# Optimization experiments

Measured on AMD Instinct MI355X. Metric: run time of the kernel, lower is better.

## Reference

```python
import jax, jax.numpy as jnp
import numpy as np

M, TS, NX, NY = 24, 60, 192, 192   # solutions, source timesteps, source grid
H, D = 4, 8                         # num_heads, d_head
SIGMA = 0.2
N_TIME_STEPS = 50
T_MAX = 200.0
LX = 100.0                          # solutions[0]['params']['Lx']
SRC_T_MAX = 200.0                   # solutions[0]['params']['t_max']
NG = 50                             # target grid resolution (hard-coded in source)


def setup_inputs():
    key = jax.random.key(0)
    ks = jax.random.split(key, 8)
    c1_preds = jax.random.normal(ks[0], (M, TS, NX, NY), jnp.float32)
    c2_preds = jax.random.normal(ks[1], (M, TS, NX, NY), jnp.float32)
    lys = 30.0 + 90.0 * jax.random.uniform(ks[2], (M,), jnp.float32)
    c_cus = 0.0029 * jax.random.uniform(ks[3], (M,), jnp.float32)
    c_nis = 0.0018 * jax.random.uniform(ks[4], (M,), jnp.float32)
    params = jnp.stack([lys, c_cus, c_nis], axis=1)  # [M,3]
    # nonuniform, sorted per-solution y grid spanning [0, Ly_m]
    base = jnp.linspace(0.0, 1.0, NY, dtype=jnp.float32) ** 1.2
    src_y = lys[:, None] * base[None, :]  # [M,NY]
    src_t_last = 100.0 + 200.0 * jax.random.uniform(ks[5], (M,), jnp.float32)
    Wq = 0.3 * jax.random.normal(ks[6], (3, H * D), jnp.float32)
    Wk = 0.3 * jax.random.normal(ks[7], (3, H * D), jnp.float32)
    bq = jnp.zeros((H * D,), jnp.float32)
    bk = jnp.zeros((H * D,), jnp.float32)
    return dict(c1_preds=c1_preds, c2_preds=c2_preds, params=params, src_y=src_y,
                src_t_last=src_t_last, Wq=Wq, bq=bq, Wk=Wk, bk=bk,
                ly_target=jnp.float32(75.0), c_cu_target=jnp.float32(0.0015),
                c_ni_target=jnp.float32(0.0009))


def _axis_interp(grid, q):
    """1-D linear interp setup. grid [G] sorted, q [P] -> (idx, frac, in_bounds)."""
    G = grid.shape[-1]
    idx = jnp.clip(jnp.searchsorted(grid, q, side='right') - 1, 0, G - 2)
    g0 = jnp.take(grid, idx)
    g1 = jnp.take(grid, idx + 1)
    frac = (q - g0) / (g1 - g0)
    inb = (q >= grid[0]) & (q <= grid[-1])  # scipy fill_value=0 outside
    return idx, frac, inb


def reference(c1_preds, c2_preds, params, src_y, src_t_last, Wq, bq, Wk, bk,
              ly_target, c_cu_target, c_ni_target):
    lys, c_cus, c_nis = params[:, 0], params[:, 1], params[:, 2]
    # normalization exactly as in the torch forward
    ly_n = (lys - 30.0) / (120.0 - 30.0)
    cu_n = c_cus / 0.0029
    ni_n = c_nis / 0.0018
    t_ly = (ly_target - 30.0) / (120.0 - 30.0)
    t_cu = c_cu_target / 0.0029
    t_ni = c_ni_target / 0.0018

    p = jnp.stack([ly_n, cu_n, ni_n], axis=1)            # [M,3]
    tgt = jnp.stack([t_ly, t_cu, t_ni])[None, :]          # [1,3]
    Q = (tgt @ Wq + bq).reshape(H, D)                     # [H,D]
    K = (p @ Wk + bk).reshape(-1, H, D)                   # [M,H,D]
    logits = jnp.einsum('mhd,hd->mh', K, Q) / jnp.sqrt(jnp.float32(D))
    attn = jax.nn.softmax(logits, axis=0).mean(axis=1)    # softmax over solutions, mean heads -> [M]

    dist2 = ((ly_n - t_ly) ** 2 + (cu_n - t_cu) ** 2 + (ni_n - t_ni) ** 2) / SIGMA ** 2
    sw = jnp.exp(-dist2 / 2.0)
    sw = sw / (sw.sum() + 1e-12)
    w = attn * sw
    w = w / (w.sum() + 1e-12)
    w = jax.lax.stop_gradient(w)  # original detaches weights before interpolation

    # ---- physics-aware interpolation ----
    times = jnp.linspace(0.0, min(SRC_T_MAX, T_MAX), N_TIME_STEPS)  # [T]
    ti = jnp.clip(jnp.round(times[:, None] / src_t_last[None, :] * (TS - 1)).astype(jnp.int32),
                  0, TS - 1)                                         # [T,M]

    src_x = jnp.linspace(0.0, LX, NX)
    qx = jnp.linspace(0.0, LX, NG)
    qy = (jnp.arange(NG, dtype=jnp.float32) / (NG - 1)) * ly_target  # linspace(0, ly_target, NG)

    ix, fx, mx = _axis_interp(src_x, qx)                             # [NG] each (shared x grid)
    scale = ly_target / lys                                           # [M]
    y_scaled = src_y * scale[:, None]                                 # [M,NY]
    iy, fy, my = jax.vmap(lambda g: _axis_interp(g, qy))(y_scaled)    # [M,NG] each
    mask = (mx[None, :, None] & my[:, None, :]).astype(c1_preds.dtype)  # [M,NG,NG]

    T = N_TIME_STEPS
    iy_b = jnp.broadcast_to(iy[None, :, None, :], (T, M, NG, NG))
    iy1_b = jnp.broadcast_to((iy + 1)[None, :, None, :], (T, M, NG, NG))

    def interp_field(preds):
        vals = preds[jnp.arange(M)[None, :], ti]                      # [T,M,NX,NY] time gather
        fxc = fx[None, None, :, None]
        vx = vals[:, :, ix, :] * (1.0 - fxc) + vals[:, :, ix + 1, :] * fxc  # [T,M,NG,NY]
        v0 = jnp.take_along_axis(vx, iy_b, axis=3)                    # [T,M,NG,NG]
        v1 = jnp.take_along_axis(vx, iy1_b, axis=3)
        fyc = fy[None, :, None, :]
        v = (v0 * (1.0 - fyc) + v1 * fyc) * mask[None]
        return jnp.einsum('tmij,m->tij', v, w)                        # weighted sum over solutions

    c1 = interp_field(c1_preds).at[:, :, 0].set(c_cu_target)
    c2 = interp_field(c2_preds).at[:, :, -1].set(c_ni_target)
    return jnp.stack([c1, c2])  # [2, T, NG, NG]
```

## Files before the change

kernel.cpp:

```cpp
#include <hip/hip_runtime.h>
#include <math.h>

#define M   24
#define TS  60
#define NX  192
#define NY  192
#define H_  4
#define D_  8
#define NTS 50
#define NG  50

__device__ float g_w[M];
__device__ int   g_ti[NTS][M];
__device__ int   g_ix[NG];
__device__ float g_fx[NG];
__device__ float g_mx[NG];
__device__ int   g_iy[M][NG];
__device__ float g_fy[M][NG];
__device__ float g_my[M][NG];

__global__ __launch_bounds__(256) void prep_kernel(
    const float* __restrict__ params, const float* __restrict__ src_y,
    const float* __restrict__ stl,
    const float* __restrict__ Wq, const float* __restrict__ bq,
    const float* __restrict__ Wk, const float* __restrict__ bk,
    const float* __restrict__ lyt_p, const float* __restrict__ ccu_p,
    const float* __restrict__ cni_p)
{
    const int tid = threadIdx.x;
    __shared__ float s_logits[M][H_];
    __shared__ float s_sw[M];

    const float ly_target = lyt_p[0];
    const float c_cu_t = ccu_p[0];
    const float c_ni_t = cni_p[0];

    const float t_ly = (ly_target - 30.0f) / 90.0f;
    const float t_cu = c_cu_t / 0.0029f;
    const float t_ni = c_ni_t / 0.0018f;

    if (tid < M) {
        const int m = tid;
        const float ly  = params[m*3 + 0];
        const float ccu = params[m*3 + 1];
        const float cni = params[m*3 + 2];
        const float ly_n = (ly - 30.0f) / 90.0f;
        const float cu_n = ccu / 0.0029f;
        const float ni_n = cni / 0.0018f;
        for (int h = 0; h < H_; ++h) {
            float acc = 0.0f;
            for (int d = 0; d < D_; ++d) {
                const int col = h*D_ + d;
                const float q = t_ly*Wq[0*32+col] + t_cu*Wq[1*32+col] + t_ni*Wq[2*32+col] + bq[col];
                const float k = ly_n*Wk[0*32+col] + cu_n*Wk[1*32+col] + ni_n*Wk[2*32+col] + bk[col];
                acc += k * q;
            }
            s_logits[m][h] = acc / sqrtf(8.0f);
        }
        const float dly = ly_n - t_ly, dcu = cu_n - t_cu, dni = ni_n - t_ni;
        const float d2 = (dly*dly + dcu*dcu + dni*dni) / 0.04f;
        s_sw[m] = expf(-d2 * 0.5f);
    }
    __syncthreads();

    if (tid == 0) {
        float attn[M];
        for (int m = 0; m < M; ++m) attn[m] = 0.0f;
        for (int h = 0; h < H_; ++h) {
            float mxv = -1e30f;
            for (int m = 0; m < M; ++m) mxv = fmaxf(mxv, s_logits[m][h]);
            float e[M]; float s = 0.0f;
            for (int m = 0; m < M; ++m) { e[m] = expf(s_logits[m][h] - mxv); s += e[m]; }
            for (int m = 0; m < M; ++m) attn[m] += e[m] / s;
        }
        float ssw = 0.0f;
        for (int m = 0; m < M; ++m) ssw += s_sw[m];
        float w[M]; float wsum = 0.0f;
        for (int m = 0; m < M; ++m) {
            w[m] = (attn[m] * 0.25f) * (s_sw[m] / (ssw + 1e-12f));
            wsum += w[m];
        }
        for (int m = 0; m < M; ++m) g_w[m] = w[m] / (wsum + 1e-12f);
    }

    const float step_t = 200.0f / 49.0f;
    for (int idx = tid; idx < NTS*M; idx += blockDim.x) {
        const int t = idx / M, m = idx % M;
        const float tt = (t == NTS-1) ? 200.0f : step_t * (float)t;
        const float r = tt / stl[m] * 59.0f;
        int ti = (int)rintf(r);
        ti = ti < 0 ? 0 : (ti > TS-1 ? TS-1 : ti);
        g_ti[t][m] = ti;
    }

    if (tid < NG) {
        const int i = tid;
        const float step_x = 100.0f / 191.0f;
        const float step_q = 100.0f / 49.0f;
        const float q = (i == NG-1) ? 100.0f : step_q * (float)i;
        int pos = 0;
        for (int g = 0; g < NX; ++g) {
            const float gv = (g == NX-1) ? 100.0f : step_x * (float)g;
            if (gv <= q) pos = g + 1;
        }
        int id = pos - 1;
        id = id < 0 ? 0 : (id > NX-2 ? NX-2 : id);
        const float g0 = (id   == NX-1) ? 100.0f : step_x * (float)id;
        const float g1 = (id+1 == NX-1) ? 100.0f : step_x * (float)(id+1);
        g_ix[i] = id;
        g_fx[i] = (q - g0) / (g1 - g0);
        g_mx[i] = (q >= 0.0f && q <= 100.0f) ? 1.0f : 0.0f;
    }

    for (int idx = tid; idx < M*NG; idx += blockDim.x) {
        const int m = idx / NG, j = idx % NG;
        const float scale = ly_target / params[m*3 + 0];
        const float q = (float)j / 49.0f * ly_target;
        const float* sy = src_y + m*NY;
        int pos = 0;
        for (int g = 0; g < NY; ++g) {
            const float gv = sy[g] * scale;
            if (gv <= q) pos = g + 1;
        }
        int id = pos - 1;
        id = id < 0 ? 0 : (id > NY-2 ? NY-2 : id);
        const float g0 = sy[id] * scale;
        const float g1 = sy[id+1] * scale;
        g_iy[m][j] = id;
        g_fy[m][j] = (q - g0) / (g1 - g0);
        const float gfirst = sy[0] * scale;
        const float glast  = sy[NY-1] * scale;
        g_my[m][j] = (q >= gfirst && q <= glast) ? 1.0f : 0.0f;
    }
}

__global__ __launch_bounds__(256) void interp_kernel(
    const float* __restrict__ c1, const float* __restrict__ c2,
    float* __restrict__ out,
    const float* __restrict__ ccu_p, const float* __restrict__ cni_p)
{
    const int p = blockIdx.x * blockDim.x + threadIdx.x;
    if (p >= NG*NG) return;
    const int t = blockIdx.y;
    const int f = blockIdx.z;
    const int i = p / NG;
    const int j = p % NG;

    const float* __restrict__ preds = (f == 0) ? c1 : c2;

    const int   ixi = g_ix[i];
    const float fxi = g_fx[i];
    const float mxi = g_mx[i];

    float acc = 0.0f;
    #pragma unroll 4
    for (int m = 0; m < M; ++m) {
        const int tim   = g_ti[t][m];
        const int iyj   = g_iy[m][j];
        const float fyj = g_fy[m][j];
        const float msk = mxi * g_my[m][j];
        const float wm  = g_w[m];
        const float* base = preds + (((size_t)m*TS + tim)*NX + ixi)*(size_t)NY + iyj;
        const float v00 = base[0];
        const float v01 = base[1];
        const float v10 = base[NY];
        const float v11 = base[NY + 1];
        const float vx0 = v00*(1.0f - fxi) + v10*fxi;
        const float vx1 = v01*(1.0f - fxi) + v11*fxi;
        const float v   = (vx0*(1.0f - fyj) + vx1*fyj) * msk;
        acc += v * wm;
    }

    if (f == 0 && j == 0)    acc = ccu_p[0];
    if (f == 1 && j == NG-1) acc = cni_p[0];

    out[(((size_t)f*NTS + t)*NG + i)*NG + j] = acc;
}

extern "C" void kernel_launch(void* const* d_in, const int* in_sizes, int n_in,
                              void* d_out, int out_size, void* d_ws, size_t ws_size,
                              hipStream_t stream) {
    const float* c1     = (const float*)d_in[0];
    const float* c2     = (const float*)d_in[1];
    const float* params = (const float*)d_in[2];
    const float* src_y  = (const float*)d_in[3];
    const float* stl    = (const float*)d_in[4];
    const float* Wq     = (const float*)d_in[5];
    const float* bq     = (const float*)d_in[6];
    const float* Wk     = (const float*)d_in[7];
    const float* bk     = (const float*)d_in[8];
    const float* lyt    = (const float*)d_in[9];
    const float* ccut   = (const float*)d_in[10];
    const float* cnit   = (const float*)d_in[11];
    float* out = (float*)d_out;

    prep_kernel<<<1, 256, 0, stream>>>(params, src_y, stl, Wq, bq, Wk, bk, lyt, ccut, cnit);

    dim3 grid((NG*NG + 255) / 256, NTS, 2);
    interp_kernel<<<grid, 256, 0, stream>>>(c1, c2, out, ccut, cnit);
}
```

Before: 410.9 us.

## Stage x-interpolated rows in shared memory per solution and reduce with atomics

Each interp block now handles one (solution, timestep, field) triple. It loads the needed pairs of x-rows with float4 loads, x-interpolates them into shared memory, then y-interpolates all 2500 output points from LDS and accumulates the weighted result into the output with atomicAdd. The output zeroing and boundary-constant writes are folded into the prep kernel as extra blocks. The aim is to replace scattered 4-point global gathers per solution with coalesced row loads and on-chip reuse. The cost is 24-way float atomic contention per output element and nondeterministic summation order.

```diff
diff --git a/kernel.cpp b/kernel.cpp
--- a/kernel.cpp
+++ b/kernel.cpp
@@ -19,15 +19,31 @@
 __device__ float g_fy[M][NG];
 __device__ float g_my[M][NG];
 
-__global__ __launch_bounds__(256) void prep_kernel(
+__global__ __launch_bounds__(256) void prep_init_kernel(
     const float* __restrict__ params, const float* __restrict__ src_y,
     const float* __restrict__ stl,
     const float* __restrict__ Wq, const float* __restrict__ bq,
     const float* __restrict__ Wk, const float* __restrict__ bk,
     const float* __restrict__ lyt_p, const float* __restrict__ ccu_p,
-    const float* __restrict__ cni_p)
+    const float* __restrict__ cni_p,
+    float* __restrict__ out)
 {
     const int tid = threadIdx.x;
+
+    if (blockIdx.x > 0) {
+        const int idx = (blockIdx.x - 1) * blockDim.x + tid;
+        const int total = 2 * NTS * NG * NG;
+        if (idx < total) {
+            const int j = idx % NG;
+            const int f = idx / (NTS * NG * NG);
+            float v = 0.0f;
+            if (f == 0 && j == 0)    v = ccu_p[0];
+            if (f == 1 && j == NG-1) v = cni_p[0];
+            out[idx] = v;
+        }
+        return;
+    }
+
     __shared__ float s_logits[M][H_];
     __shared__ float s_sw[M];
 
@@ -136,45 +152,46 @@
 
 __global__ __launch_bounds__(256) void interp_kernel(
     const float* __restrict__ c1, const float* __restrict__ c2,
-    float* __restrict__ out,
-    const float* __restrict__ ccu_p, const float* __restrict__ cni_p)
+    float* __restrict__ out)
 {
-    const int p = blockIdx.x * blockDim.x + threadIdx.x;
-    if (p >= NG*NG) return;
+    const int m = blockIdx.x;
     const int t = blockIdx.y;
     const int f = blockIdx.z;
-    const int i = p / NG;
-    const int j = p % NG;
+    const int tid = threadIdx.x;
+
+    __shared__ float xrow[NG][NY + 1];
 
     const float* __restrict__ preds = (f == 0) ? c1 : c2;
-
-    const int   ixi = g_ix[i];
-    const float fxi = g_fx[i];
-    const float mxi = g_mx[i];
-
-    float acc = 0.0f;
-    #pragma unroll 4
-    for (int m = 0; m < M; ++m) {
-        const int tim   = g_ti[t][m];
-        const int iyj   = g_iy[m][j];
+    const int tim = g_ti[t][m];
+    const float* __restrict__ slice = preds + (((size_t)m * TS + tim) * NX) * (size_t)NY;
+
+    for (int idx = tid; idx < NG * (NY / 4); idx += blockDim.x) {
+        const int i  = idx / (NY / 4);
+        const int y4 = (idx - i * (NY / 4)) * 4;
+        const int   ixi = g_ix[i];
+        const float fxi = g_fx[i];
+        const float4 r0 = *(const float4*)(slice + (size_t)ixi * NY + y4);
+        const float4 r1 = *(const float4*)(slice + (size_t)(ixi + 1) * NY + y4);
+        xrow[i][y4 + 0] = r0.x * (1.0f - fxi) + r1.x * fxi;
+        xrow[i][y4 + 1] = r0.y * (1.0f - fxi) + r1.y * fxi;
+        xrow[i][y4 + 2] = r0.z * (1.0f - fxi) + r1.z * fxi;
+        xrow[i][y4 + 3] = r0.w * (1.0f - fxi) + r1.w * fxi;
+    }
+    __syncthreads();
+
+    const float wm = g_w[m];
+    for (int idx = tid; idx < NG * NG; idx += blockDim.x) {
+        const int i = idx / NG;
+        const int j = idx - i * NG;
+        if ((f == 0 && j == 0) || (f == 1 && j == NG - 1)) continue;
+        const int   iyj = g_iy[m][j];
         const float fyj = g_fy[m][j];
-        const float msk = mxi * g_my[m][j];
-        const float wm  = g_w[m];
-        const float* base = preds + (((size_t)m*TS + tim)*NX + ixi)*(size_t)NY + iyj;
-        const float v00 = base[0];
-        const float v01 = base[1];
-        const float v10 = base[NY];
-        const float v11 = base[NY + 1];
-        const float vx0 = v00*(1.0f - fxi) + v10*fxi;
-        const float vx1 = v01*(1.0f - fxi) + v11*fxi;
-        const float v   = (vx0*(1.0f - fyj) + vx1*fyj) * msk;
-        acc += v * wm;
-    }
-
-    if (f == 0 && j == 0)    acc = ccu_p[0];
-    if (f == 1 && j == NG-1) acc = cni_p[0];
-
-    out[(((size_t)f*NTS + t)*NG + i)*NG + j] = acc;
+        const float msk = g_mx[i] * g_my[m][j];
+        const float v0 = xrow[i][iyj];
+        const float v1 = xrow[i][iyj + 1];
+        const float v = (v0 * (1.0f - fyj) + v1 * fyj) * msk;
+        atomicAdd(&out[(((size_t)f * NTS + t) * NG + i) * NG + j], v * wm);
+    }
 }
 
 extern "C" void kernel_launch(void* const* d_in, const int* in_sizes, int n_in,
@@ -194,8 +211,11 @@
     const float* cnit   = (const float*)d_in[11];
     float* out = (float*)d_out;
 
-    prep_kernel<<<1, 256, 0, stream>>>(params, src_y, stl, Wq, bq, Wk, bk, lyt, ccut, cnit);
-
-    dim3 grid((NG*NG + 255) / 256, NTS, 2);
-    interp_kernel<<<grid, 256, 0, stream>>>(c1, c2, out, ccut, cnit);
+    const int total = 2 * NTS * NG * NG;
+    const int init_blocks = (total + 255) / 256;
+    prep_init_kernel<<<1 + init_blocks, 256, 0, stream>>>(
+        params, src_y, stl, Wq, bq, Wk, bk, lyt, ccut, cnit, out);
+
+    dim3 grid(M, NTS, 2);
+    interp_kernel<<<grid, 256, 0, stream>>>(c1, c2, out);
 }
```

New measurement: 436.8 us. 1.06x slower.
